# Kernel tuning notes

Hardware: AMD Instinct MI355X
Metric: run time of the kernel (lower is better)

The kernel has to match this reference:

```python
import jax, jax.numpy as jnp
import numpy as np

B, C, H, W = 4, 256, 64, 64
CH = C // 2


def setup_inputs() -> dict:
    key = jax.random.key(0)
    ks = jax.random.split(key, 8)
    s_in = 1.0 / np.sqrt(C)  # conv2d default init scale (fan_in = C for 1x1)
    return {
        "a": jax.random.normal(ks[0], (B, C, H, W), dtype=jnp.float32),
        "p": jax.random.normal(ks[1], (B, C, H, W), dtype=jnp.float32),
        "Wq": jax.random.uniform(ks[2], (CH, C), jnp.float32, -s_in, s_in),
        "bq": jax.random.uniform(ks[3], (CH,), jnp.float32, -s_in, s_in),
        "Wk": jax.random.uniform(ks[4], (CH, C), jnp.float32, -s_in, s_in),
        "bk": jax.random.uniform(ks[5], (CH,), jnp.float32, -s_in, s_in),
        "Wv": jax.random.uniform(ks[6], (C, C), jnp.float32, -s_in, s_in),
        "bv": jax.random.uniform(ks[7], (C,), jnp.float32, -s_in, s_in),
    }


def reference(a, p, Wq, bq, Wk, bk, Wv, bv):
    b, c, h, w = a.shape
    hw = h * w
    # 1x1 convs == per-pixel channel matmuls; flatten spatial dims to hw
    Q = jnp.einsum('oc,bchw->bohw', Wq, a).reshape(b, -1, hw) + bq[None, :, None]   # [B, C/2, HW]
    K = jnp.einsum('oc,bchw->bohw', Wk, p).reshape(b, -1, hw) + bk[None, :, None]   # [B, C/2, HW]
    V = jnp.einsum('oc,bchw->bohw', Wv, p).reshape(b, -1, hw) + bv[None, :, None]   # [B, C,   HW]
    # attn[b,m,n] = softmax_n( Q[:, :, m] . K[:, :, n] )
    attn = jax.nn.softmax(jnp.einsum('bcm,bcn->bmn', Q, K), axis=-1)                # [B, HW, HW]
    # out[b,c,m] = sum_n V[b,c,n] * attn[b,m,n]  (V @ attn^T)
    out = jnp.einsum('bcn,bmn->bcm', V, attn).reshape(b, c, h, w)
    return out + a
```

## Files before the change

kernel.cpp:

```cpp
#include <hip/hip_runtime.h>
#include <stdint.h>

#define B_ 4
#define C_ 256
#define CH_ 128
#define HW_ 4096
#define L2E 1.44269504f
#define SHIFT_L2 14.4269504f

typedef __bf16 bf16;
typedef __bf16 v8bf __attribute__((ext_vector_type(8)));
typedef float v4f __attribute__((ext_vector_type(4)));
struct f4 { float x, y, z, w; };

#define GAS __attribute__((address_space(1)))
#define LAS __attribute__((address_space(3)))

__device__ __forceinline__ void async_copy16(const void* gptr, void* lptr) {
  __builtin_amdgcn_global_load_lds((GAS void*)gptr, (LAS void*)lptr, 16, 0, 0);
}

__global__ __launch_bounds__(512)
void proj_kernel(const float* __restrict__ a, const float* __restrict__ p,
                 const float* __restrict__ Wq, const float* __restrict__ bq,
                 const float* __restrict__ Wk, const float* __restrict__ bk,
                 const float* __restrict__ Wv, const float* __restrict__ bv,
                 bf16* __restrict__ Qt, bf16* __restrict__ Kt, bf16* __restrict__ Vn)
{
  __shared__ bf16 Xt[64 * 266];
  __shared__ bf16 Ds[9600];

  const int t = threadIdx.x;
  const int lane = t & 63;
  const int w = t >> 6;
  const int l15 = lane & 15;
  const int q = lane >> 4;

  const int s0 = blockIdx.x * 64;
  const int b = blockIdx.y;
  const int z = blockIdx.z;

  const float* X = (z == 0) ? a : p;
  const float* W; const float* bias;
  if (z == 0)      { W = Wq; bias = bq; }
  else if (z == 1) { W = Wk; bias = bk; }
  else             { W = Wv + (size_t)(z - 2) * 128 * C_; bias = bv + (z - 2) * 128; }

  const float* Xb = X + ((size_t)b * C_) * HW_;
  for (int j = 0; j < 16; ++j) {
    int linear = t + 512 * j;
    int s = linear & 63;
    int cp = linear >> 6;
    float x0 = Xb[(size_t)(2 * cp) * HW_ + s0 + s];
    float x1 = Xb[(size_t)(2 * cp + 1) * HW_ + s0 + s];
    unsigned short u0 = __builtin_bit_cast(unsigned short, (bf16)x0);
    unsigned short u1 = __builtin_bit_cast(unsigned short, (bf16)x1);
    *(unsigned int*)&Xt[s * 266 + 2 * cp] = (unsigned int)u0 | ((unsigned int)u1 << 16);
  }

  v8bf Af[8];
  const float* Wrow = W + (size_t)(16 * w + l15) * C_;
  #pragma unroll
  for (int kk = 0; kk < 8; ++kk) {
    f4 f0 = *(const f4*)&Wrow[kk * 32 + q * 8];
    f4 f1 = *(const f4*)&Wrow[kk * 32 + q * 8 + 4];
    v8bf f;
    f[0] = (bf16)f0.x; f[1] = (bf16)f0.y; f[2] = (bf16)f0.z; f[3] = (bf16)f0.w;
    f[4] = (bf16)f1.x; f[5] = (bf16)f1.y; f[6] = (bf16)f1.z; f[7] = (bf16)f1.w;
    Af[kk] = f;
  }

  __syncthreads();

  v4f acc[4];
  #pragma unroll
  for (int ns = 0; ns < 4; ++ns) { v4f zz = {0.f, 0.f, 0.f, 0.f}; acc[ns] = zz; }
  #pragma unroll
  for (int ns = 0; ns < 4; ++ns)
    #pragma unroll
    for (int kk = 0; kk < 8; ++kk) {
      v8bf Bf = *(const v8bf*)&Xt[(16 * ns + l15) * 266 + kk * 32 + q * 8];
      acc[ns] = __builtin_amdgcn_mfma_f32_16x16x32_bf16(Af[kk], Bf, acc[ns], 0, 0, 0);
    }

  if (z < 2) {
    #pragma unroll
    for (int ns = 0; ns < 4; ++ns)
      #pragma unroll
      for (int r = 0; r < 4; ++r)
        Ds[(16 * ns + l15) * 150 + 16 * w + 4 * q + r] =
            (bf16)(acc[ns][r] + bias[16 * w + 4 * q + r]);
    __syncthreads();
    bf16* dst = (z == 0) ? Qt : Kt;
    #pragma unroll
    for (int i = 0; i < 2; ++i) {
      int idx = t + 512 * i;
      int s = idx >> 4, ch = (idx & 15) * 8;
      *(v8bf*)&dst[((size_t)b * HW_ + s0 + s) * CH_ + ch] = *(const v8bf*)&Ds[s * 150 + ch];
    }
  } else {
    int o0 = (z - 2) * 128;
    #pragma unroll
    for (int ns = 0; ns < 4; ++ns)
      #pragma unroll
      for (int r = 0; r < 4; ++r) {
        int pos = 32 * (ns >> 1) + 8 * (l15 >> 2) + 4 * (ns & 1) + (l15 & 3);
        Ds[(16 * w + 4 * q + r) * 72 + pos] =
            (bf16)(acc[ns][r] + bias[16 * w + 4 * q + r]);
      }
    __syncthreads();
    #pragma unroll
    for (int i = 0; i < 2; ++i) {
      int idx = t + 512 * i;
      int o = idx >> 3, ch = (idx & 7) * 8;
      *(v8bf*)&Vn[((size_t)b * C_ + o0 + o) * HW_ + s0 + ch] = *(const v8bf*)&Ds[o * 72 + ch];
    }
  }
}

#define LDS_V 16640
#define LDS_TOTAL 49920

__global__ __launch_bounds__(256, 2)
void attn_kernel(const bf16* __restrict__ Qt, const bf16* __restrict__ Kt,
                 const bf16* __restrict__ Vn, const float* __restrict__ a,
                 float* __restrict__ out, bf16* __restrict__ Op,
                 float* __restrict__ Ls, int nsplit)
{
  extern __shared__ char smem[];
  const int t = threadIdx.x;
  const int lane = t & 63;
  const int w = t >> 6;
  const int l15 = lane & 15;
  const int q = lane >> 4;
  const int b = blockIdx.y;
  const int sp = blockIdx.z;
  const int m0 = blockIdx.x * 128;

  v8bf Qf[2][4];
  #pragma unroll
  for (int s = 0; s < 2; ++s) {
    const bf16* qrow = Qt + ((size_t)b * HW_ + m0 + 32 * w + 16 * s + l15) * CH_;
    #pragma unroll
    for (int kk = 0; kk < 4; ++kk)
      Qf[s][kk] = *(const v8bf*)&qrow[kk * 32 + q * 8];
  }

  v4f O[2][16];
  #pragma unroll
  for (int s = 0; s < 2; ++s)
    #pragma unroll
    for (int cs = 0; cs < 16; ++cs) { v4f zz = {0.f, 0.f, 0.f, 0.f}; O[s][cs] = zz; }
  float lsum[2] = {0.f, 0.f};

  const bf16* Kb = Kt + (size_t)b * HW_ * CH_;
  const bf16* Vb = Vn + (size_t)b * C_ * HW_;

  const int NT = 64 / nsplit;
  const int t0 = sp * NT;

  auto stageK = [&](int n0) {
    #pragma unroll
    for (int j = 0; j < 4; ++j) {
      int i = 4 * j + w;
      async_copy16(Kb + ((size_t)(n0 + i + 16 * q)) * CH_ + l15 * 8, smem + i * 1040);
    }
  };
  auto stageV = [&](int n0) {
    #pragma unroll
    for (int j = 0; j < 8; ++j) {
      int i = 4 * j + w;
      async_copy16(Vb + ((size_t)(i + 32 * (lane >> 3))) * HW_ + n0 + (lane & 7) * 8,
                   smem + LDS_V + i * 1040);
    }
  };

  stageK(t0 * 64);
  stageV(t0 * 64);
  __syncthreads();

  for (int nt = 0; nt < NT; ++nt) {
    int n0 = (t0 + nt) * 64;

    v4f St[4][2];
    #pragma unroll
    for (int sub = 0; sub < 4; ++sub)
      #pragma unroll
      for (int s = 0; s < 2; ++s) { v4f zz = {0.f, 0.f, 0.f, 0.f}; St[sub][s] = zz; }
    #pragma unroll
    for (int sub = 0; sub < 4; ++sub)
      #pragma unroll
      for (int kk = 0; kk < 4; ++kk) {
        v8bf Kf = *(const v8bf*)(smem + l15 * 1040 + sub * 256 + kk * 64 + q * 16);
        St[sub][0] = __builtin_amdgcn_mfma_f32_16x16x32_bf16(Kf, Qf[0][kk], St[sub][0], 0, 0, 0);
        St[sub][1] = __builtin_amdgcn_mfma_f32_16x16x32_bf16(Kf, Qf[1][kk], St[sub][1], 0, 0, 0);
      }

    __syncthreads();
    if (nt + 1 < NT) stageK(n0 + 64);

    v8bf Pf[2][2];
    #pragma unroll
    for (int s = 0; s < 2; ++s) {
      float ls = 0.f;
      #pragma unroll
      for (int kk = 0; kk < 2; ++kk)
        #pragma unroll
        for (int a2 = 0; a2 < 2; ++a2)
          #pragma unroll
          for (int r = 0; r < 4; ++r) {
            float pv = exp2f(St[2 * kk + a2][s][r] * L2E - SHIFT_L2);
            Pf[s][kk][4 * a2 + r] = (bf16)pv;
            ls += pv;
          }
      lsum[s] += ls;
    }

    #pragma unroll
    for (int cs = 0; cs < 16; ++cs)
      #pragma unroll
      for (int kk = 0; kk < 2; ++kk) {
        v8bf Vf = *(const v8bf*)(smem + LDS_V +
                                 (16 * (cs & 1) + l15) * 1040 + (cs >> 1) * 128 + kk * 64 + q * 16);
        O[0][cs] = __builtin_amdgcn_mfma_f32_16x16x32_bf16(Pf[0][kk], Vf, O[0][cs], 0, 0, 0);
        O[1][cs] = __builtin_amdgcn_mfma_f32_16x16x32_bf16(Pf[1][kk], Vf, O[1][cs], 0, 0, 0);
      }

    __syncthreads();
    if (nt + 1 < NT) stageV(n0 + 64);
  }

  float lfin[2];
  #pragma unroll
  for (int s = 0; s < 2; ++s) {
    float l = lsum[s];
    l += __shfl_xor(l, 16);
    l += __shfl_xor(l, 32);
    lfin[s] = l;
  }

  if (nsplit > 1 && lane < 16) {
    #pragma unroll
    for (int s = 0; s < 2; ++s)
      Ls[((size_t)sp * B_ + b) * HW_ + m0 + 32 * w + 16 * s + lane] = lfin[s];
  }

  float linv[2][4];
  #pragma unroll
  for (int s = 0; s < 2; ++s)
    #pragma unroll
    for (int r = 0; r < 4; ++r)
      linv[s][r] = (nsplit == 1) ? 1.0f / __shfl(lfin[s], 4 * q + r) : 1.0f;

  bf16* T = (bf16*)smem;
  for (int round = 0; round < 2; ++round) {
    __syncthreads();
    if ((w >> 1) == round) {
      bf16* Tw = T + (w & 1) * 12288;
      #pragma unroll
      for (int s = 0; s < 2; ++s)
        #pragma unroll
        for (int cs = 0; cs < 16; ++cs)
          #pragma unroll
          for (int r = 0; r < 4; ++r)
            Tw[(16 * cs + l15) * 48 + 16 * s + 4 * q + r] = (bf16)(O[s][cs][r] * linv[s][r]);
    }
    __syncthreads();
    #pragma unroll
    for (int it = 0; it < 8; ++it) {
      int idx = t + 256 * it;
      int tt = idx >> 10;
      int c = (idx >> 2) & 255;
      int mc = idx & 3;
      int wavew = round * 2 + tt;
      int mg = m0 + 32 * wavew + mc * 8;
      v8bf val = *(const v8bf*)&T[tt * 12288 + c * 48 + mc * 8];
      if (nsplit == 1) {
        size_t gi = ((size_t)b * C_ + c) * HW_ + mg;
        #pragma unroll
        for (int j2 = 0; j2 < 8; ++j2) out[gi + j2] = (float)val[j2] + a[gi + j2];
      } else {
        size_t gi = (((size_t)sp * B_ + b) * C_ + c) * HW_ + mg;
        *(v8bf*)&Op[gi] = val;
      }
    }
  }
}

__global__ __launch_bounds__(256)
void combine_kernel(const bf16* __restrict__ Op, const float* __restrict__ Ls,
                    const float* __restrict__ a, float* __restrict__ out, int nsplit)
{
  int idx = blockIdx.x * 256 + threadIdx.x;
  int m8 = (idx & (HW_ / 8 - 1)) * 8;
  int bc = idx >> 9;
  int b = bc >> 8;

  float acc[8], L[8];
  #pragma unroll
  for (int j = 0; j < 8; ++j) { acc[j] = 0.f; L[j] = 0.f; }
  for (int s = 0; s < nsplit; ++s) {
    v8bf o = *(const v8bf*)&Op[((size_t)s * B_ * C_ + bc) * HW_ + m8];
    const float* lp = Ls + ((size_t)s * B_ + b) * HW_ + m8;
    #pragma unroll
    for (int j = 0; j < 8; ++j) { acc[j] += (float)o[j]; L[j] += lp[j]; }
  }
  const float* ap = a + (size_t)bc * HW_ + m8;
  float* op = out + (size_t)bc * HW_ + m8;
  #pragma unroll
  for (int j = 0; j < 8; ++j) op[j] = acc[j] / L[j] + ap[j];
}

extern "C" void kernel_launch(void* const* d_in, const int* in_sizes, int n_in,
                              void* d_out, int out_size, void* d_ws, size_t ws_size,
                              hipStream_t stream) {
  const float* a  = (const float*)d_in[0];
  const float* p  = (const float*)d_in[1];
  const float* Wq = (const float*)d_in[2];
  const float* bq = (const float*)d_in[3];
  const float* Wk = (const float*)d_in[4];
  const float* bk = (const float*)d_in[5];
  const float* Wv = (const float*)d_in[6];
  const float* bv = (const float*)d_in[7];
  float* out = (float*)d_out;

  bf16* Qt = (bf16*)d_ws;
  bf16* Kt = Qt + (size_t)B_ * HW_ * CH_;
  bf16* Vn = Kt + (size_t)B_ * HW_ * CH_;

  const size_t proj_bytes = 16777216ull;
  const size_t part_bytes = (size_t)B_ * C_ * HW_ * 2;
  const size_t stat_bytes = (size_t)B_ * HW_ * 4;
  auto need = [&](int S) { return proj_bytes + (size_t)S * (part_bytes + stat_bytes); };

  int S;
  if      (ws_size >= need(4)) S = 4;
  else if (ws_size >= need(2)) S = 2;
  else                         S = 1;

  bf16* Op = (bf16*)((char*)d_ws + proj_bytes);
  float* Ls = (float*)((char*)d_ws + proj_bytes + (size_t)S * part_bytes);

  dim3 pg(HW_ / 64, B_, 4);
  proj_kernel<<<pg, 512, 0, stream>>>(a, p, Wq, bq, Wk, bk, Wv, bv, Qt, Kt, Vn);

  dim3 ag(HW_ / 128, B_, S);
  attn_kernel<<<ag, 256, LDS_TOTAL, stream>>>(Qt, Kt, Vn, a, out, Op, Ls, S);

  if (S > 1) {
    int nblk = (B_ * C_ * HW_ / 8) / 256;
    combine_kernel<<<nblk, 256, 0, stream>>>(Op, Ls, a, out, S);
  }
}
```

Baseline: 176.2 us.

## Double-buffer K tiles and interleave next QK^T with current PV MFMAs

Adds a second LDS buffer for K so the next tile's score MFMAs can be interleaved with the current tile's P·V MFMAs, software-pipelining the attention loop. The first score tile is computed before the loop, and the K prefetch now runs two tiles ahead. The aim is to keep the matrix units busy across the softmax and barrier phases and to hide K load latency. In exchange, the kernel uses more LDS (about 66 KB per block), holds the St accumulators live across iterations, which raises register pressure, and has more complex buffer indexing.

```diff
diff --git a/kernel.cpp b/kernel.cpp
--- a/kernel.cpp
+++ b/kernel.cpp
@@ -118,8 +118,8 @@
   }
 }
 
-#define LDS_V 16640
-#define LDS_TOTAL 49920
+#define LDS_V 33280
+#define LDS_TOTAL 66560
 
 __global__ __launch_bounds__(256, 2)
 void attn_kernel(const bf16* __restrict__ Qt, const bf16* __restrict__ Kt,
@@ -159,11 +159,12 @@
   const int NT = 64 / nsplit;
   const int t0 = sp * NT;
 
-  auto stageK = [&](int n0) {
+  auto stageK = [&](int buf, int n0) {
+    char* kbase = smem + buf * 16640;
     #pragma unroll
     for (int j = 0; j < 4; ++j) {
       int i = 4 * j + w;
-      async_copy16(Kb + ((size_t)(n0 + i + 16 * q)) * CH_ + l15 * 8, smem + i * 1040);
+      async_copy16(Kb + ((size_t)(n0 + i + 16 * q)) * CH_ + l15 * 8, kbase + i * 1040);
     }
   };
   auto stageV = [&](int n0) {
@@ -175,29 +176,27 @@
     }
   };
 
-  stageK(t0 * 64);
+  stageK(0, t0 * 64);
   stageV(t0 * 64);
   __syncthreads();
 
+  v4f St[4][2];
+  #pragma unroll
+  for (int sub = 0; sub < 4; ++sub)
+    #pragma unroll
+    for (int s = 0; s < 2; ++s) { v4f zz = {0.f, 0.f, 0.f, 0.f}; St[sub][s] = zz; }
+  #pragma unroll
+  for (int sub = 0; sub < 4; ++sub)
+    #pragma unroll
+    for (int kk = 0; kk < 4; ++kk) {
+      v8bf Kf = *(const v8bf*)(smem + l15 * 1040 + sub * 256 + kk * 64 + q * 16);
+      St[sub][0] = __builtin_amdgcn_mfma_f32_16x16x32_bf16(Kf, Qf[0][kk], St[sub][0], 0, 0, 0);
+      St[sub][1] = __builtin_amdgcn_mfma_f32_16x16x32_bf16(Kf, Qf[1][kk], St[sub][1], 0, 0, 0);
+    }
+  if (NT > 1) stageK(1, t0 * 64 + 64);
+
   for (int nt = 0; nt < NT; ++nt) {
-    int n0 = (t0 + nt) * 64;
-
-    v4f St[4][2];
-    #pragma unroll
-    for (int sub = 0; sub < 4; ++sub)
-      #pragma unroll
-      for (int s = 0; s < 2; ++s) { v4f zz = {0.f, 0.f, 0.f, 0.f}; St[sub][s] = zz; }
-    #pragma unroll
-    for (int sub = 0; sub < 4; ++sub)
-      #pragma unroll
-      for (int kk = 0; kk < 4; ++kk) {
-        v8bf Kf = *(const v8bf*)(smem + l15 * 1040 + sub * 256 + kk * 64 + q * 16);
-        St[sub][0] = __builtin_amdgcn_mfma_f32_16x16x32_bf16(Kf, Qf[0][kk], St[sub][0], 0, 0, 0);
-        St[sub][1] = __builtin_amdgcn_mfma_f32_16x16x32_bf16(Kf, Qf[1][kk], St[sub][1], 0, 0, 0);
-      }
-
-    __syncthreads();
-    if (nt + 1 < NT) stageK(n0 + 64);
+    const bool has_next = (nt + 1 < NT);
 
     v8bf Pf[2][2];
     #pragma unroll
@@ -216,18 +215,38 @@
       lsum[s] += ls;
     }
 
-    #pragma unroll
-    for (int cs = 0; cs < 16; ++cs)
-      #pragma unroll
-      for (int kk = 0; kk < 2; ++kk) {
-        v8bf Vf = *(const v8bf*)(smem + LDS_V +
-                                 (16 * (cs & 1) + l15) * 1040 + (cs >> 1) * 128 + kk * 64 + q * 16);
-        O[0][cs] = __builtin_amdgcn_mfma_f32_16x16x32_bf16(Pf[0][kk], Vf, O[0][cs], 0, 0, 0);
-        O[1][cs] = __builtin_amdgcn_mfma_f32_16x16x32_bf16(Pf[1][kk], Vf, O[1][cs], 0, 0, 0);
+    __syncthreads();
+
+    const char* knext = smem + ((nt + 1) & 1) * 16640;
+    if (has_next) {
+      #pragma unroll
+      for (int sub = 0; sub < 4; ++sub)
+        #pragma unroll
+        for (int s = 0; s < 2; ++s) { v4f zz = {0.f, 0.f, 0.f, 0.f}; St[sub][s] = zz; }
+    }
+    #pragma unroll
+    for (int i = 0; i < 16; ++i) {
+      v8bf Vf0 = *(const v8bf*)(smem + LDS_V +
+                                (16 * (i & 1) + l15) * 1040 + (i >> 1) * 128 + q * 16);
+      v8bf Vf1 = *(const v8bf*)(smem + LDS_V +
+                                (16 * (i & 1) + l15) * 1040 + (i >> 1) * 128 + 64 + q * 16);
+      O[0][i] = __builtin_amdgcn_mfma_f32_16x16x32_bf16(Pf[0][0], Vf0, O[0][i], 0, 0, 0);
+      O[1][i] = __builtin_amdgcn_mfma_f32_16x16x32_bf16(Pf[1][0], Vf0, O[1][i], 0, 0, 0);
+      O[0][i] = __builtin_amdgcn_mfma_f32_16x16x32_bf16(Pf[0][1], Vf1, O[0][i], 0, 0, 0);
+      O[1][i] = __builtin_amdgcn_mfma_f32_16x16x32_bf16(Pf[1][1], Vf1, O[1][i], 0, 0, 0);
+      if (has_next) {
+        int sub = i >> 2, kk = i & 3;
+        v8bf Kf = *(const v8bf*)(knext + l15 * 1040 + sub * 256 + kk * 64 + q * 16);
+        St[sub][0] = __builtin_amdgcn_mfma_f32_16x16x32_bf16(Kf, Qf[0][kk], St[sub][0], 0, 0, 0);
+        St[sub][1] = __builtin_amdgcn_mfma_f32_16x16x32_bf16(Kf, Qf[1][kk], St[sub][1], 0, 0, 0);
       }
-
-    __syncthreads();
+    }
+
+    __syncthreads();
+
+    int n0 = (t0 + nt) * 64;
     if (nt + 1 < NT) stageV(n0 + 64);
+    if (nt + 2 < NT) stageK(nt & 1, n0 + 128);
   }
 
   float lfin[2];
```

Result: slower. 233.8 us (+32.7%).
